# Kernel optimization log

Measured on AMD Instinct MI355X. Metric: run time of the kernel, lower is better.

Reference implementation:

```python
import jax, jax.numpy as jnp
import numpy as np


def _mlp(x, w1, b1, w2, b2, w3, b3):
    h = jax.nn.relu(x @ w1 + b1)
    h = jax.nn.relu(h @ w2 + b2)
    return h @ w3 + b3


def setup_inputs() -> dict:
    key = jax.random.key(0)
    N, E, G = 200000, 6400000, 1000
    IN, D = 16, 16
    ks = jax.random.split(key, 32)
    inp = {
        'x': jax.random.normal(ks[0], (N, IN), jnp.float32),
        'edge_index': jax.random.randint(ks[1], (2, E), 0, N),
        'batch': jnp.sort(jax.random.randint(ks[2], (N,), 0, G)),
        'num_graphs': G,
    }
    k = 3
    # make_mlp(in_ch, out_ch): in -> 32 -> 16 -> out
    for name, fin, dims in [('mlp1', IN, [32, 16, 8]),
                            ('mlp2', 8, [32, 16, D]),
                            ('mlp_dag', IN + D, [32, 16, D]),
                            ('mlp_global', D, [32, 16, D])]:
        d_in = fin
        for j, d_out in enumerate(dims):
            inp[f'{name}_w{j+1}'] = jax.random.normal(ks[k], (d_in, d_out), jnp.float32) / np.sqrt(d_in)
            inp[f'{name}_b{j+1}'] = jnp.zeros((d_out,), jnp.float32)
            k += 1
            d_in = d_out
    return inp


def reference(x, edge_index, batch, num_graphs,
              mlp1_w1, mlp1_b1, mlp1_w2, mlp1_b2, mlp1_w3, mlp1_b3,
              mlp2_w1, mlp2_b1, mlp2_w2, mlp2_b2, mlp2_w3, mlp2_b3,
              mlp_dag_w1, mlp_dag_b1, mlp_dag_w2, mlp_dag_b2, mlp_dag_w3, mlp_dag_b3,
              mlp_global_w1, mlp_global_b1, mlp_global_w2, mlp_global_b2, mlp_global_w3, mlp_global_b3):
    N = x.shape[0]
    loops = jnp.arange(N)
    row = jnp.concatenate([edge_index[0], loops])  # aggregation index (flow=target_to_source)
    col = jnp.concatenate([edge_index[1], loops])  # message source index

    # GCNConv: mlp1 -> normalized scatter-add -> mlp2
    h = _mlp(x, mlp1_w1, mlp1_b1, mlp1_w2, mlp1_b2, mlp1_w3, mlp1_b3)  # [N, 8]
    deg = jax.ops.segment_sum(jnp.ones_like(col, x.dtype), col, num_segments=N)
    dinv = jnp.where(deg > 0, 1.0 / jnp.sqrt(jnp.maximum(deg, 1.0)), 0.0)
    norm = dinv[row] * dinv[col]  # [E+N]
    agg = jax.ops.segment_sum(norm[:, None] * h[col], row, num_segments=N)  # [N, 8]
    x_node = _mlp(agg, mlp2_w1, mlp2_b1, mlp2_w2, mlp2_b2, mlp2_w3, mlp2_b3)  # [N, D]

    # DAG-level embedding: global_add_pool over batch, then mlp_dag
    x_comb = jnp.concatenate([x, x_node], axis=1)  # [N, IN+D]
    y = jax.ops.segment_sum(x_comb, batch, num_segments=num_graphs)  # [G, IN+D]
    y = _mlp(y, mlp_dag_w1, mlp_dag_b1, mlp_dag_w2, mlp_dag_b2, mlp_dag_w3, mlp_dag_b3)  # [G, D]

    # Global embedding
    z = _mlp(jnp.sum(y, axis=0), mlp_global_w1, mlp_global_b1, mlp_global_w2, mlp_global_b2, mlp_global_w3, mlp_global_b3)  # [D]
    return x_node, y, z
```

## Files before the change

### kernel.cpp

```cpp
#include <hip/hip_runtime.h>
#include <hip/hip_fp16.h>


#define BSH 8
#define BSZ 256
#define NBMAX 1024
#define TSZ 4096
#define ATSZ 8192
#define CH 16

__device__ __forceinline__ int lowerb(const int* __restrict__ b, int n, int v) {
  int lo = 0, hi = n;
  while (lo < hi) { int m = (lo + hi) >> 1; if (b[m] < v) lo = m + 1; else hi = m; }
  return lo;
}

__device__ __forceinline__ void addmsg(float* acc, uint4 g) {
  const __half2* h2 = reinterpret_cast<const __half2*>(&g);
  #pragma unroll
  for (int q = 0; q < 4; q++) {
    float2 f = __half22float2(h2[q]);
    acc[2 * q] += f.x;
    acc[2 * q + 1] += f.y;
  }
}


__global__ void __launch_bounds__(256)
k_hist(const int* __restrict__ row, const int* __restrict__ col, int E,
       int NBP, unsigned* __restrict__ Hr, unsigned* __restrict__ Hc) {
  __shared__ unsigned hr[NBMAX], hc[NBMAX];
  int t = threadIdx.x;
  int base = blockIdx.x * TSZ;
  int cnt = min(TSZ, E - base);
  for (int i = t; i < NBP; i += 256) { hr[i] = 0; hc[i] = 0; }
  __syncthreads();
  #pragma unroll
  for (int u = 0; u < 4; u++) {
    int idx = base + 4 * (t + 256 * u);
    unsigned rv[4], cv[4];
    if (idx + 3 < E) {
      uint4 r4 = *reinterpret_cast<const uint4*>(row + idx);
      uint4 c4 = *reinterpret_cast<const uint4*>(col + idx);
      rv[0] = r4.x; rv[1] = r4.y; rv[2] = r4.z; rv[3] = r4.w;
      cv[0] = c4.x; cv[1] = c4.y; cv[2] = c4.z; cv[3] = c4.w;
    } else {
      #pragma unroll
      for (int j = 0; j < 4; j++) {
        bool v = (idx + j) < E;
        rv[j] = v ? (unsigned)row[idx + j] : 0u;
        cv[j] = v ? (unsigned)col[idx + j] : 0u;
      }
    }
    int l0 = 4 * (t + 256 * u);
    #pragma unroll
    for (int j = 0; j < 4; j++) {
      if (l0 + j < cnt) {
        atomicAdd(&hr[rv[j] >> BSH], 1u);
        atomicAdd(&hc[cv[j] >> BSH], 1u);
      }
    }
  }
  __syncthreads();
  size_t rb = (size_t)blockIdx.x * NBP;
  for (int i = t; i < NBP; i += 256) {
    Hr[rb + i] = hr[i];
    Hc[rb + i] = hc[i];
  }
}

__global__ void __launch_bounds__(256)
k_colsum2(const unsigned* __restrict__ Hr, unsigned* __restrict__ Sr,
          const unsigned* __restrict__ Hc, unsigned* __restrict__ Sc,
          int NT, int NBP, int CSZ, int gcol) {
  int blk = blockIdx.x;
  const unsigned* H = Hr; unsigned* S = Sr;
  if (blk >= gcol) { blk -= gcol; H = Hc; S = Sc; }
  int i = blk * 256 + threadIdx.x;
  if (i >= CH * NBP) return;
  int ch = i / NBP, b = i - ch * NBP;
  int t0 = ch * CSZ, t1 = min(NT, t0 + CSZ);
  unsigned s = 0;
  for (int t = t0; t < t1; t++) s += H[(size_t)t * NBP + b];
  S[i] = s;
}

__global__ void __launch_bounds__(256)
k_colapply2(unsigned* __restrict__ Hr, const unsigned* __restrict__ Sr,
            unsigned* __restrict__ tot_r,
            unsigned* __restrict__ Hc, const unsigned* __restrict__ Sc,
            unsigned* __restrict__ tot_c,
            int NT, int NBP, int nb, int CSZ, int gcol) {
  int blk = blockIdx.x;
  unsigned* H = Hr; const unsigned* S = Sr; unsigned* tot = tot_r;
  if (blk >= gcol) { blk -= gcol; H = Hc; S = Sc; tot = tot_c; }
  int i = blk * 256 + threadIdx.x;
  if (i >= CH * NBP) return;
  int ch = i / NBP, b = i - ch * NBP;
  unsigned run = 0;
  for (int c = 0; c < ch; c++) run += S[c * NBP + b];
  int t0 = ch * CSZ, t1 = min(NT, t0 + CSZ);
  for (int t = t0; t < t1; t++) {
    unsigned v = H[(size_t)t * NBP + b];
    H[(size_t)t * NBP + b] = run;
    run += v;
  }
  if (ch == CH - 1 && b < nb) tot[b] = run;
}

__global__ void __launch_bounds__(1024)
k_scan2(const unsigned* __restrict__ tot_r, unsigned* __restrict__ offs_r,
        const unsigned* __restrict__ tot_c, unsigned* __restrict__ offs_c,
        int nb) {
  const unsigned* tot = blockIdx.x ? tot_c : tot_r;
  unsigned* offs = blockIdx.x ? offs_c : offs_r;
  unsigned pm1 = blockIdx.x ? 0u : 3u;
  __shared__ unsigned s[1024];
  int t = threadIdx.x;
  unsigned e0 = (2 * t < nb) ? ((tot[2 * t] + pm1) & ~pm1) : 0u;
  unsigned e1 = (2 * t + 1 < nb) ? ((tot[2 * t + 1] + pm1) & ~pm1) : 0u;
  unsigned sum = e0 + e1;
  s[t] = sum;
  __syncthreads();
  for (int d = 1; d < 1024; d <<= 1) {
    unsigned v = (t >= d) ? s[t - d] : 0u;
    __syncthreads();
    s[t] += v;
    __syncthreads();
  }
  unsigned ex = s[t] - sum;
  if (2 * t < nb)     offs[2 * t] = ex;
  if (2 * t + 1 < nb) offs[2 * t + 1] = ex + e0;
}

__global__ void __launch_bounds__(256)
k_scat2(const int* __restrict__ row, const int* __restrict__ col, int E, int nb,
        int NBP,
        const unsigned* __restrict__ Hr, const unsigned* __restrict__ Hc,
        const unsigned* __restrict__ offs_r, const unsigned* __restrict__ offs_c,
        unsigned* __restrict__ ebuf, unsigned short* __restrict__ ebuf2) {
  __shared__ unsigned buf[TSZ];
  __shared__ unsigned short bkt[TSZ];
  __shared__ unsigned h[NBMAX], diff[NBMAX];
  __shared__ unsigned sc[256];
  int t = threadIdx.x;
  int base = blockIdx.x * TSZ;
  int cnt = min(TSZ, E - base);
  size_t hrow = (size_t)blockIdx.x * NBP;

  unsigned rv[16], cv[16];
  #pragma unroll
  for (int u = 0; u < 4; u++) {
    int idx = base + 4 * (t + 256 * u);
    if (idx + 3 < E) {
      uint4 r4 = *reinterpret_cast<const uint4*>(row + idx);
      uint4 c4 = *reinterpret_cast<const uint4*>(col + idx);
      rv[4*u] = r4.x; rv[4*u+1] = r4.y; rv[4*u+2] = r4.z; rv[4*u+3] = r4.w;
      cv[4*u] = c4.x; cv[4*u+1] = c4.y; cv[4*u+2] = c4.z; cv[4*u+3] = c4.w;
    } else {
      #pragma unroll
      for (int j = 0; j < 4; j++) {
        bool v = (idx + j) < E;
        rv[4*u+j] = v ? (unsigned)row[idx + j] : 0u;
        cv[4*u+j] = v ? (unsigned)col[idx + j] : 0u;
      }
    }
  }

  for (int i = t; i < NBMAX; i += 256) h[i] = 0;
  __syncthreads();
  unsigned rk[16];
  #pragma unroll
  for (int u = 0; u < 4; u++) {
    int l0 = 4 * (t + 256 * u);
    #pragma unroll
    for (int j = 0; j < 4; j++)
      if (l0 + j < cnt) rk[4*u+j] = atomicAdd(&h[rv[4*u+j] >> BSH], 1u);
  }
  __syncthreads();
  {
    unsigned a0 = h[4*t], a1 = h[4*t+1], a2 = h[4*t+2], a3 = h[4*t+3];
    unsigned p1 = a0 + a1, p2 = p1 + a2, p3 = p2 + a3;
    sc[t] = p3;
    __syncthreads();
    for (int d = 1; d < 256; d <<= 1) {
      unsigned v = (t >= d) ? sc[t - d] : 0u;
      __syncthreads();
      sc[t] += v;
      __syncthreads();
    }
    unsigned ex = sc[t] - p3;
    unsigned l[4] = {ex, ex + a0, ex + p1, ex + p2};
    #pragma unroll
    for (int k = 0; k < 4; k++) {
      int b = 4 * t + k;
      h[b] = l[k];
      if (b < nb) diff[b] = offs_r[b] + Hr[hrow + b] - l[k];
    }
  }
  __syncthreads();
  #pragma unroll
  for (int u = 0; u < 4; u++) {
    int l0 = 4 * (t + 256 * u);
    #pragma unroll
    for (int j = 0; j < 4; j++) {
      if (l0 + j < cnt) {
        unsigned r = rv[4*u+j], b = r >> BSH;
        unsigned pos = h[b] + rk[4*u+j];
        buf[pos] = ((r & (BSZ - 1u)) << 18) | cv[4*u+j];
        bkt[pos] = (unsigned short)b;
      }
    }
  }
  __syncthreads();
  #pragma unroll
  for (int u = 0; u < 16; u++) {
    int s2 = t + 256 * u;
    if (s2 < cnt) {
      ebuf[(unsigned)s2 + diff[bkt[s2]]] = buf[s2];
    }
  }
  __syncthreads();

  for (int i = t; i < NBMAX; i += 256) h[i] = 0;
  __syncthreads();
  #pragma unroll
  for (int u = 0; u < 4; u++) {
    int l0 = 4 * (t + 256 * u);
    #pragma unroll
    for (int j = 0; j < 4; j++)
      if (l0 + j < cnt) rk[4*u+j] = atomicAdd(&h[cv[4*u+j] >> BSH], 1u);
  }
  __syncthreads();
  {
    unsigned a0 = h[4*t], a1 = h[4*t+1], a2 = h[4*t+2], a3 = h[4*t+3];
    unsigned p1 = a0 + a1, p2 = p1 + a2, p3 = p2 + a3;
    sc[t] = p3;
    __syncthreads();
    for (int d = 1; d < 256; d <<= 1) {
      unsigned v = (t >= d) ? sc[t - d] : 0u;
      __syncthreads();
      sc[t] += v;
      __syncthreads();
    }
    unsigned ex = sc[t] - p3;
    unsigned l[4] = {ex, ex + a0, ex + p1, ex + p2};
    #pragma unroll
    for (int k = 0; k < 4; k++) {
      int b = 4 * t + k;
      h[b] = l[k];
      if (b < nb) diff[b] = offs_c[b] + Hc[hrow + b] - l[k];
    }
  }
  __syncthreads();
  #pragma unroll
  for (int u = 0; u < 4; u++) {
    int l0 = 4 * (t + 256 * u);
    #pragma unroll
    for (int j = 0; j < 4; j++) {
      if (l0 + j < cnt) {
        unsigned c = cv[4*u+j], b = c >> BSH;
        unsigned pos = h[b] + rk[4*u+j];
        buf[pos] = c & (BSZ - 1u);
        bkt[pos] = (unsigned short)b;
      }
    }
  }
  __syncthreads();
  #pragma unroll
  for (int u = 0; u < 16; u++) {
    int s2 = t + 256 * u;
    if (s2 < cnt) {
      ebuf2[(unsigned)s2 + diff[bkt[s2]]] = (unsigned short)buf[s2];
    }
  }
}


__global__ void __launch_bounds__(256)
k_degm(const unsigned short* __restrict__ eb, const unsigned* __restrict__ offs_c,
       const unsigned* __restrict__ tot_c,
       const float* __restrict__ x,
       const float* __restrict__ w1, const float* __restrict__ b1,
       const float* __restrict__ w2, const float* __restrict__ b2,
       const float* __restrict__ w3, const float* __restrict__ b3,
       unsigned* __restrict__ deg, uint4* __restrict__ hs16, int N) {
  __shared__ unsigned cnt[BSZ];
  __shared__ float sW1[16 * 32], sB1[32], sW2[32 * 16], sB2[16], sW3[16 * 8], sB3[8];
  int b = blockIdx.x, t = threadIdx.x;
  cnt[t] = 0;
  sW1[t] = w1[t]; sW1[t + 256] = w1[t + 256];
  sW2[t] = w2[t]; sW2[t + 256] = w2[t + 256];
  if (t < 128) sW3[t] = w3[t];
  if (t < 32) sB1[t] = b1[t];
  if (t < 16) sB2[t] = b2[t];
  if (t < 8) sB3[t] = b3[t];
  __syncthreads();
  unsigned s = offs_c[b], n = tot_c[b];
  for (unsigned i = t; i < n; i += 256) atomicAdd(&cnt[eb[s + i]], 1u);
  __syncthreads();
  int node = b * BSZ + t;
  if (node >= N) return;
  unsigned d = cnt[t];
  deg[node] = d;

  float xin[16];
  const float4* xp = reinterpret_cast<const float4*>(x + (size_t)node * 16);
  #pragma unroll
  for (int q = 0; q < 4; q++) {
    float4 v = xp[q];
    xin[q * 4 + 0] = v.x; xin[q * 4 + 1] = v.y; xin[q * 4 + 2] = v.z; xin[q * 4 + 3] = v.w;
  }
  float h1[32];
  #pragma unroll
  for (int o = 0; o < 32; o++) {
    float s1 = sB1[o];
    #pragma unroll
    for (int k = 0; k < 16; k++) s1 = fmaf(xin[k], sW1[k * 32 + o], s1);
    h1[o] = fmaxf(s1, 0.f);
  }
  float h2[16];
  #pragma unroll
  for (int o = 0; o < 16; o++) {
    float s1 = sB2[o];
    #pragma unroll
    for (int k = 0; k < 32; k++) s1 = fmaf(h1[k], sW2[k * 16 + o], s1);
    h2[o] = fmaxf(s1, 0.f);
  }
  float dinv = rsqrtf((float)(d + 1u));
  float o0[8];
  #pragma unroll
  for (int o = 0; o < 8; o++) {
    float s1 = sB3[o];
    #pragma unroll
    for (int k = 0; k < 16; k++) s1 = fmaf(h2[k], sW3[k * 8 + o], s1);
    o0[o] = dinv * s1;
  }
  __half2 hh[4];
  #pragma unroll
  for (int q = 0; q < 4; q++) hh[q] = __floats2half2_rn(o0[2 * q], o0[2 * q + 1]);
  hs16[node] = *reinterpret_cast<const uint4*>(hh);
}


__global__ void __launch_bounds__(512)
k_agg(const unsigned* __restrict__ ebuf, const unsigned* __restrict__ offs,
      const unsigned* __restrict__ tot,
      const uint4* __restrict__ hs16, const unsigned* __restrict__ deg,
      const float* __restrict__ w1, const float* __restrict__ b1,
      const float* __restrict__ w2, const float* __restrict__ b2,
      const float* __restrict__ w3, const float* __restrict__ b3,
      float* __restrict__ xn, int N) {
  __shared__ unsigned sorted[ATSZ];
  __shared__ unsigned hist[256];
  __shared__ unsigned cum[257];
  __shared__ unsigned sc[256];
  __shared__ float stage[BSZ][9];
  __shared__ float sW1[256], sB1[32], sW2[512], sB2[16], sW3[256], sB3[16];
  int t = threadIdx.x;
  if (t < 256) { sW1[t] = w1[t]; sW3[t] = w3[t]; }
  else { int u = t - 256; sW2[u] = w2[u]; sW2[u + 256] = w2[u + 256]; }
  if (t < 32) sB1[t] = b1[t];
  if (t < 16) { sB2[t] = b2[t]; sB3[t] = b3[t]; }

  int b = blockIdx.x;
  unsigned s = offs[b], n = tot[b];
  unsigned nr = (n + 3u) & ~3u;

  float acc[8];
  #pragma unroll
  for (int c = 0; c < 8; c++) acc[c] = 0.f;
  int nl = t >> 1, half = t & 1;

  for (unsigned c0 = 0; c0 < n; c0 += ATSZ) {
    if (t < 256) hist[t] = 0;
    __syncthreads();

    unsigned rel[16], colv[16], rk[16];
    #pragma unroll
    for (int u = 0; u < 4; u++) {
      unsigned idx = c0 + 4 * (unsigned)(t + 512 * u);
      uint4 pk = make_uint4(0u, 0u, 0u, 0u);
      if (idx < nr) pk = *reinterpret_cast<const uint4*>(ebuf + s + idx);
      #pragma unroll
      for (int j = 0; j < 4; j++) {
        bool real = (idx + j) < n;
        unsigned p = (&pk.x)[j];
        rel[4*u+j]  = real ? (p >> 18) : 256u;
        colv[4*u+j] = p & 0x3FFFFu;
      }
    }
    #pragma unroll
    for (int u = 0; u < 16; u++)
      if (rel[u] < 256u) rk[u] = atomicAdd(&hist[rel[u]], 1u);
    __syncthreads();
    if (t < 256) sc[t] = hist[t];
    __syncthreads();
    for (int d = 1; d < 256; d <<= 1) {
      unsigned v = (t >= d && t < 256) ? sc[t - d] : 0u;
      __syncthreads();
      if (t < 256) sc[t] += v;
      __syncthreads();
    }
    if (t < 256) cum[t] = sc[t] - hist[t];
    if (t == 255) cum[256] = sc[255];
    __syncthreads();
    #pragma unroll
    for (int u = 0; u < 16; u++) {
      if (rel[u] < 256u) {
        sorted[cum[rel[u]] + rk[u]] = colv[u];
      }
    }
    __syncthreads();
    unsigned lo = cum[nl], hi = cum[nl + 1];
    unsigned len = hi - lo, mid = lo + (len >> 1);
    unsigned i = half ? mid : lo;
    unsigned e = half ? hi : mid;
    for (; i + 4 <= e; i += 4) {
      unsigned q0 = sorted[i], q1 = sorted[i + 1], q2 = sorted[i + 2], q3 = sorted[i + 3];
      uint4 g0 = hs16[q0];
      uint4 g1 = hs16[q1];
      uint4 g2 = hs16[q2];
      uint4 g3 = hs16[q3];
      addmsg(acc, g0); addmsg(acc, g1); addmsg(acc, g2); addmsg(acc, g3);
    }
    for (; i < e; i++) { uint4 g = hs16[sorted[i]]; addmsg(acc, g); }
    __syncthreads();
  }

  if (!half) {
    #pragma unroll
    for (int c = 0; c < 8; c++) stage[nl][c] = acc[c];
  }
  __syncthreads();
  if (half) {
    #pragma unroll
    for (int c = 0; c < 8; c++) stage[nl][c] += acc[c];
  }
  __syncthreads();

  if (t >= 256) return;
  int node = b * BSZ + t;
  if (node >= N) return;
  float dinv = rsqrtf((float)(deg[node] + 1u));
  uint4 selfp = hs16[node];
  const __half2* sh = reinterpret_cast<const __half2*>(&selfp);
  float a[8];
  #pragma unroll
  for (int q = 0; q < 4; q++) {
    float2 f = __half22float2(sh[q]);
    a[2 * q]     = dinv * (stage[t][2 * q] + f.x);
    a[2 * q + 1] = dinv * (stage[t][2 * q + 1] + f.y);
  }

  float h1[32];
  #pragma unroll
  for (int o = 0; o < 32; o++) {
    float v = sB1[o];
    #pragma unroll
    for (int k = 0; k < 8; k++) v = fmaf(a[k], sW1[k * 32 + o], v);
    h1[o] = fmaxf(v, 0.f);
  }
  float h2v[16];
  #pragma unroll
  for (int o = 0; o < 16; o++) {
    float v = sB2[o];
    #pragma unroll
    for (int k = 0; k < 32; k++) v = fmaf(h1[k], sW2[k * 16 + o], v);
    h2v[o] = fmaxf(v, 0.f);
  }
  float o0[16];
  #pragma unroll
  for (int o = 0; o < 16; o++) {
    float v = sB3[o];
    #pragma unroll
    for (int k = 0; k < 16; k++) v = fmaf(h2v[k], sW3[k * 16 + o], v);
    o0[o] = v;
  }
  float4* op = reinterpret_cast<float4*>(xn + (size_t)node * 16);
  #pragma unroll
  for (int q = 0; q < 4; q++)
    op[q] = make_float4(o0[q * 4], o0[q * 4 + 1], o0[q * 4 + 2], o0[q * 4 + 3]);
}


__global__ void __launch_bounds__(256)
k_pool(const float* __restrict__ x, const float* __restrict__ xn,
       const int* __restrict__ batch, float* __restrict__ pool, int N) {
  int g = blockIdx.x;
  int lo = lowerb(batch, N, g);
  int hi = lowerb(batch, N, g + 1);
  int c = threadIdx.x & 31;
  int j = threadIdx.x >> 5;
  float s = 0.f;
  for (int n = lo + j; n < hi; n += 8) {
    s += (c < 16) ? x[(size_t)n * 16 + c] : xn[(size_t)n * 16 + (c - 16)];
  }
  __shared__ float red[8][33];
  red[j][c] = s;
  __syncthreads();
  if (threadIdx.x < 32) {
    float t = 0.f;
    #pragma unroll
    for (int q = 0; q < 8; q++) t += red[q][threadIdx.x];
    pool[(size_t)g * 32 + threadIdx.x] = t;
  }
}

__global__ void __launch_bounds__(256)
k_dag(const float* __restrict__ pool,
      const float* __restrict__ w1, const float* __restrict__ b1,
      const float* __restrict__ w2, const float* __restrict__ b2,
      const float* __restrict__ w3, const float* __restrict__ b3,
      float* __restrict__ y, int G) {
  __shared__ float sW1[32 * 32], sB1[32], sW2[32 * 16], sB2[16], sW3[16 * 16], sB3[16];
  for (int t = threadIdx.x; t < 1024; t += blockDim.x) sW1[t] = w1[t];
  for (int t = threadIdx.x; t < 512; t += blockDim.x) sW2[t] = w2[t];
  for (int t = threadIdx.x; t < 256; t += blockDim.x) sW3[t] = w3[t];
  for (int t = threadIdx.x; t < 32; t += blockDim.x) sB1[t] = b1[t];
  for (int t = threadIdx.x; t < 16; t += blockDim.x) { sB2[t] = b2[t]; sB3[t] = b3[t]; }
  __syncthreads();
  int g = blockIdx.x * blockDim.x + threadIdx.x;
  if (g >= G) return;

  float in[32];
  const float4* pp = reinterpret_cast<const float4*>(pool + (size_t)g * 32);
  #pragma unroll
  for (int q = 0; q < 8; q++) {
    float4 v = pp[q];
    in[q * 4 + 0] = v.x; in[q * 4 + 1] = v.y; in[q * 4 + 2] = v.z; in[q * 4 + 3] = v.w;
  }
  float h1[32];
  #pragma unroll
  for (int o = 0; o < 32; o++) {
    float s = sB1[o];
    #pragma unroll
    for (int k = 0; k < 32; k++) s = fmaf(in[k], sW1[k * 32 + o], s);
    h1[o] = fmaxf(s, 0.f);
  }
  float h2[16];
  #pragma unroll
  for (int o = 0; o < 16; o++) {
    float s = sB2[o];
    #pragma unroll
    for (int k = 0; k < 32; k++) s = fmaf(h1[k], sW2[k * 16 + o], s);
    h2[o] = fmaxf(s, 0.f);
  }
  float o0[16];
  #pragma unroll
  for (int o = 0; o < 16; o++) {
    float s = sB3[o];
    #pragma unroll
    for (int k = 0; k < 16; k++) s = fmaf(h2[k], sW3[k * 16 + o], s);
    o0[o] = s;
  }
  float4* yp = reinterpret_cast<float4*>(y + (size_t)g * 16);
  #pragma unroll
  for (int q = 0; q < 4; q++)
    yp[q] = make_float4(o0[q * 4], o0[q * 4 + 1], o0[q * 4 + 2], o0[q * 4 + 3]);
}

__global__ void __launch_bounds__(256)
k_z(const float* __restrict__ y,
    const float* __restrict__ w1, const float* __restrict__ b1,
    const float* __restrict__ w2, const float* __restrict__ b2,
    const float* __restrict__ w3, const float* __restrict__ b3,
    float* __restrict__ z, int G) {
  __shared__ float red[16][17];
  __shared__ float sum[16], h1s[32], h2s[16];
  int t = threadIdx.x;
  int c = t & 15, j = t >> 4;
  float s = 0.f;
  for (int g = j; g < G; g += 16) s += y[(size_t)g * 16 + c];
  red[j][c] = s;
  __syncthreads();
  if (t < 16) {
    float v = 0.f;
    #pragma unroll
    for (int q = 0; q < 16; q++) v += red[q][t];
    sum[t] = v;
  }
  __syncthreads();
  if (t < 32) {
    float s1 = b1[t];
    #pragma unroll
    for (int k = 0; k < 16; k++) s1 = fmaf(sum[k], w1[k * 32 + t], s1);
    h1s[t] = fmaxf(s1, 0.f);
  }
  __syncthreads();
  if (t < 16) {
    float s2 = b2[t];
    #pragma unroll
    for (int k = 0; k < 32; k++) s2 = fmaf(h1s[k], w2[k * 16 + t], s2);
    h2s[t] = fmaxf(s2, 0.f);
  }
  __syncthreads();
  if (t < 16) {
    float s3 = b3[t];
    #pragma unroll
    for (int k = 0; k < 16; k++) s3 = fmaf(h2s[k], w3[k * 16 + t], s3);
    z[t] = s3;
  }
}


__global__ void k_deg_atomic(const int* __restrict__ col, unsigned* __restrict__ deg, int E) {
  int e = blockIdx.x * blockDim.x + threadIdx.x;
  if (e < E) atomicAdd(&deg[col[e]], 1u);
}

__global__ void __launch_bounds__(256)
k_mlp1f(const float* __restrict__ x, const unsigned* __restrict__ deg,
        const float* __restrict__ w1, const float* __restrict__ b1,
        const float* __restrict__ w2, const float* __restrict__ b2,
        const float* __restrict__ w3, const float* __restrict__ b3,
        float* __restrict__ hs, int N) {
  __shared__ float sW1[16 * 32], sB1[32], sW2[32 * 16], sB2[16], sW3[16 * 8], sB3[8];
  for (int t = threadIdx.x; t < 512; t += blockDim.x) { sW1[t] = w1[t]; sW2[t] = w2[t]; }
  for (int t = threadIdx.x; t < 128; t += blockDim.x) sW3[t] = w3[t];
  for (int t = threadIdx.x; t < 32; t += blockDim.x) sB1[t] = b1[t];
  for (int t = threadIdx.x; t < 16; t += blockDim.x) sB2[t] = b2[t];
  for (int t = threadIdx.x; t < 8; t += blockDim.x) sB3[t] = b3[t];
  __syncthreads();
  int i = blockIdx.x * blockDim.x + threadIdx.x;
  if (i >= N) return;
  float xin[16];
  const float4* xp = reinterpret_cast<const float4*>(x + (size_t)i * 16);
  #pragma unroll
  for (int q = 0; q < 4; q++) {
    float4 v = xp[q];
    xin[q * 4 + 0] = v.x; xin[q * 4 + 1] = v.y; xin[q * 4 + 2] = v.z; xin[q * 4 + 3] = v.w;
  }
  float h1[32];
  #pragma unroll
  for (int o = 0; o < 32; o++) {
    float s = sB1[o];
    #pragma unroll
    for (int k = 0; k < 16; k++) s = fmaf(xin[k], sW1[k * 32 + o], s);
    h1[o] = fmaxf(s, 0.f);
  }
  float h2[16];
  #pragma unroll
  for (int o = 0; o < 16; o++) {
    float s = sB2[o];
    #pragma unroll
    for (int k = 0; k < 32; k++) s = fmaf(h1[k], sW2[k * 16 + o], s);
    h2[o] = fmaxf(s, 0.f);
  }
  float dinv = rsqrtf((float)(deg[i] + 1u));
  float o0[8];
  #pragma unroll
  for (int o = 0; o < 8; o++) {
    float s = sB3[o];
    #pragma unroll
    for (int k = 0; k < 16; k++) s = fmaf(h2[k], sW3[k * 8 + o], s);
    o0[o] = dinv * s;
  }
  float4* hp = reinterpret_cast<float4*>(hs + (size_t)i * 8);
  hp[0] = make_float4(o0[0], o0[1], o0[2], o0[3]);
  hp[1] = make_float4(o0[4], o0[5], o0[6], o0[7]);
}

__global__ void k_scatter_atomic(const int* __restrict__ row, const int* __restrict__ col,
                                 const float* __restrict__ hs, float* __restrict__ acc, int E) {
  int e = blockIdx.x * blockDim.x + threadIdx.x;
  if (e >= E) return;
  int r = row[e], c = col[e];
  const float4* hp = reinterpret_cast<const float4*>(hs + (size_t)c * 8);
  float4 a = hp[0], b = hp[1];
  float* ap = acc + (size_t)r * 8;
  atomicAdd(ap + 0, a.x); atomicAdd(ap + 1, a.y);
  atomicAdd(ap + 2, a.z); atomicAdd(ap + 3, a.w);
  atomicAdd(ap + 4, b.x); atomicAdd(ap + 5, b.y);
  atomicAdd(ap + 6, b.z); atomicAdd(ap + 7, b.w);
}

__global__ void __launch_bounds__(256)
k_finalize(const float* __restrict__ hs, const float* __restrict__ acc,
           const unsigned* __restrict__ deg,
           const float* __restrict__ w1, const float* __restrict__ b1,
           const float* __restrict__ w2, const float* __restrict__ b2,
           const float* __restrict__ w3, const float* __restrict__ b3,
           float* __restrict__ xn, int N) {
  __shared__ float sW1[8 * 32], sB1[32], sW2[32 * 16], sB2[16], sW3[16 * 16], sB3[16];
  for (int t = threadIdx.x; t < 256; t += blockDim.x) { sW1[t] = w1[t]; sW3[t] = w3[t]; }
  for (int t = threadIdx.x; t < 512; t += blockDim.x) sW2[t] = w2[t];
  for (int t = threadIdx.x; t < 32; t += blockDim.x) sB1[t] = b1[t];
  for (int t = threadIdx.x; t < 16; t += blockDim.x) { sB2[t] = b2[t]; sB3[t] = b3[t]; }
  __syncthreads();
  int i = blockIdx.x * blockDim.x + threadIdx.x;
  if (i >= N) return;
  float dinv = rsqrtf((float)(deg[i] + 1u));
  float a[8];
  const float4* accp = reinterpret_cast<const float4*>(acc + (size_t)i * 8);
  const float4* hsp = reinterpret_cast<const float4*>(hs + (size_t)i * 8);
  float4 a0 = accp[0], a1 = accp[1], s0 = hsp[0], s1 = hsp[1];
  a[0] = dinv * (a0.x + s0.x); a[1] = dinv * (a0.y + s0.y);
  a[2] = dinv * (a0.z + s0.z); a[3] = dinv * (a0.w + s0.w);
  a[4] = dinv * (a1.x + s1.x); a[5] = dinv * (a1.y + s1.y);
  a[6] = dinv * (a1.z + s1.z); a[7] = dinv * (a1.w + s1.w);
  float h1[32];
  #pragma unroll
  for (int o = 0; o < 32; o++) {
    float s = sB1[o];
    #pragma unroll
    for (int k = 0; k < 8; k++) s = fmaf(a[k], sW1[k * 32 + o], s);
    h1[o] = fmaxf(s, 0.f);
  }
  float h2[16];
  #pragma unroll
  for (int o = 0; o < 16; o++) {
    float s = sB2[o];
    #pragma unroll
    for (int k = 0; k < 32; k++) s = fmaf(h1[k], sW2[k * 16 + o], s);
    h2[o] = fmaxf(s, 0.f);
  }
  float o0[16];
  #pragma unroll
  for (int o = 0; o < 16; o++) {
    float s = sB3[o];
    #pragma unroll
    for (int k = 0; k < 16; k++) s = fmaf(h2[k], sW3[k * 16 + o], s);
    o0[o] = s;
  }
  float4* op = reinterpret_cast<float4*>(xn + (size_t)i * 16);
  #pragma unroll
  for (int q = 0; q < 4; q++)
    op[q] = make_float4(o0[q * 4], o0[q * 4 + 1], o0[q * 4 + 2], o0[q * 4 + 3]);
}


extern "C" void kernel_launch(void* const* d_in, const int* in_sizes, int n_in,
                              void* d_out, int out_size, void* d_ws, size_t ws_size,
                              hipStream_t stream) {
  const float* x = (const float*)d_in[0];
  const int* ei = (const int*)d_in[1];
  const int* batch = (const int*)d_in[2];
  const float* m1w1 = (const float*)d_in[4];  const float* m1b1 = (const float*)d_in[5];
  const float* m1w2 = (const float*)d_in[6];  const float* m1b2 = (const float*)d_in[7];
  const float* m1w3 = (const float*)d_in[8];  const float* m1b3 = (const float*)d_in[9];
  const float* m2w1 = (const float*)d_in[10]; const float* m2b1 = (const float*)d_in[11];
  const float* m2w2 = (const float*)d_in[12]; const float* m2b2 = (const float*)d_in[13];
  const float* m2w3 = (const float*)d_in[14]; const float* m2b3 = (const float*)d_in[15];
  const float* mdw1 = (const float*)d_in[16]; const float* mdb1 = (const float*)d_in[17];
  const float* mdw2 = (const float*)d_in[18]; const float* mdb2 = (const float*)d_in[19];
  const float* mdw3 = (const float*)d_in[20]; const float* mdb3 = (const float*)d_in[21];
  const float* mgw1 = (const float*)d_in[22]; const float* mgb1 = (const float*)d_in[23];
  const float* mgw2 = (const float*)d_in[24]; const float* mgb2 = (const float*)d_in[25];
  const float* mgw3 = (const float*)d_in[26]; const float* mgb3 = (const float*)d_in[27];

  int N = in_sizes[0] / 16;
  int E = in_sizes[1] / 2;
  int G = (out_size - N * 16 - 16) / 16;
  const int* rowp = ei;
  const int* colp = ei + E;

  float* xn = (float*)d_out;
  float* yv = xn + (size_t)N * 16;
  float* zv = yv + (size_t)G * 16;

  int nb = (N + BSZ - 1) / BSZ;
  int NT = (E + TSZ - 1) / TSZ;
  int NBP = (nb + 63) & ~63;
  int CSZ = (NT + CH - 1) / CH;

  size_t off = 0;
  auto alloc = [&](size_t bytes) -> size_t {
    off = (off + 255) & ~(size_t)255;
    size_t o = off; off += bytes; return o;
  };
  char* ws = (char*)d_ws;
  size_t o_deg  = alloc((size_t)N * 4);
  size_t o_hs16 = alloc((size_t)N * 16);
  size_t o_cnt  = alloc((size_t)4 * NBMAX * 4);
  size_t o_Hr   = alloc((size_t)NT * NBP * 4);
  size_t o_Hc   = alloc((size_t)NT * NBP * 4);
  size_t o_S    = alloc((size_t)2 * CH * NBP * 4);
  size_t o_eb   = alloc(((size_t)E + 4 * NBMAX) * 4);
  size_t o_eb2  = alloc((size_t)E * 2);
  size_t o_pool = alloc((size_t)G * 32 * 4);
  size_t need = off;

  bool bucketed = (ws_size >= need) && (nb <= NBMAX) && (N <= (1 << 18));

  if (bucketed) {
    unsigned* deg = (unsigned*)(ws + o_deg);
    uint4* hs16 = (uint4*)(ws + o_hs16);
    unsigned* tot_r  = (unsigned*)(ws + o_cnt);
    unsigned* offs_r = tot_r + NBMAX;
    unsigned* tot_c  = tot_r + 2 * NBMAX;
    unsigned* offs_c = tot_r + 3 * NBMAX;
    unsigned* Hr = (unsigned*)(ws + o_Hr);
    unsigned* Hc = (unsigned*)(ws + o_Hc);
    unsigned* Sr = (unsigned*)(ws + o_S);
    unsigned* Sc = Sr + CH * NBP;
    unsigned* ebuf = (unsigned*)(ws + o_eb);
    unsigned short* ebuf2 = (unsigned short*)(ws + o_eb2);
    float* pool = (float*)(ws + o_pool);

    int gcol = (CH * NBP + 255) / 256;
    k_hist<<<NT, 256, 0, stream>>>(rowp, colp, E, NBP, Hr, Hc);
    k_colsum2<<<2 * gcol, 256, 0, stream>>>(Hr, Sr, Hc, Sc, NT, NBP, CSZ, gcol);
    k_colapply2<<<2 * gcol, 256, 0, stream>>>(Hr, Sr, tot_r, Hc, Sc, tot_c,
                                              NT, NBP, nb, CSZ, gcol);
    k_scan2<<<2, 1024, 0, stream>>>(tot_r, offs_r, tot_c, offs_c, nb);
    k_scat2<<<NT, 256, 0, stream>>>(rowp, colp, E, nb, NBP, Hr, Hc,
                                    offs_r, offs_c, ebuf, ebuf2);
    k_degm<<<nb, 256, 0, stream>>>(ebuf2, offs_c, tot_c, x,
                                   m1w1, m1b1, m1w2, m1b2, m1w3, m1b3,
                                   deg, hs16, N);
    k_agg<<<nb, 512, 0, stream>>>(ebuf, offs_r, tot_r, hs16, deg,
                                  m2w1, m2b1, m2w2, m2b2, m2w3, m2b3, xn, N);

    k_pool<<<G, 256, 0, stream>>>(x, xn, batch, pool, N);
    k_dag<<<(G + 255) / 256, 256, 0, stream>>>(pool, mdw1, mdb1, mdw2, mdb2, mdw3, mdb3, yv, G);
    k_z<<<1, 256, 0, stream>>>(yv, mgw1, mgb1, mgw2, mgb2, mgw3, mgb3, zv, G);
  } else {
    unsigned* deg = (unsigned*)ws;
    float* acc = (float*)(ws + (size_t)N * 4);
    float* hs  = (float*)(ws + (size_t)N * 36);
    float* pool = (float*)(ws + (size_t)N * 68);

    hipMemsetAsync(ws, 0, (size_t)N * 36, stream);
    const int TB = 256;
    k_deg_atomic<<<(E + TB - 1) / TB, TB, 0, stream>>>(colp, deg, E);
    k_mlp1f<<<(N + TB - 1) / TB, TB, 0, stream>>>(x, deg, m1w1, m1b1, m1w2, m1b2, m1w3, m1b3, hs, N);
    k_scatter_atomic<<<(E + TB - 1) / TB, TB, 0, stream>>>(rowp, colp, hs, acc, E);
    k_finalize<<<(N + TB - 1) / TB, TB, 0, stream>>>(hs, acc, deg, m2w1, m2b1, m2w2, m2b2, m2w3, m2b3, xn, N);
    k_pool<<<G, TB, 0, stream>>>(x, xn, batch, pool, N);
    k_dag<<<(G + TB - 1) / TB, TB, 0, stream>>>(pool, mdw1, mdb1, mdw2, mdb2, mdw3, mdb3, yv, G);
    k_z<<<1, TB, 0, stream>>>(yv, mgw1, mgb1, mgw2, mgb2, mgw3, mgb3, zv, G);
  }
}
```

Before: 243.2 us.

## Widen scatter blocks, use wave-shuffle scans, balance aggregation, fuse pool with DAG MLP

Result: slower. 283.2 us (+16.5%).

```diff
diff --git a/kernel.cpp b/kernel.cpp
--- a/kernel.cpp
+++ b/kernel.cpp
@@ -133,7 +133,7 @@
   if (2 * t + 1 < nb) offs[2 * t + 1] = ex + e0;
 }
 
-__global__ void __launch_bounds__(256)
+__global__ void __launch_bounds__(512)
 k_scat2(const int* __restrict__ row, const int* __restrict__ col, int E, int nb,
         int NBP,
         const unsigned* __restrict__ Hr, const unsigned* __restrict__ Hc,
@@ -142,16 +142,16 @@
   __shared__ unsigned buf[TSZ];
   __shared__ unsigned short bkt[TSZ];
   __shared__ unsigned h[NBMAX], diff[NBMAX];
-  __shared__ unsigned sc[256];
+  __shared__ unsigned wtot[4];
   int t = threadIdx.x;
   int base = blockIdx.x * TSZ;
   int cnt = min(TSZ, E - base);
   size_t hrow = (size_t)blockIdx.x * NBP;
 
-  unsigned rv[16], cv[16];
-  #pragma unroll
-  for (int u = 0; u < 4; u++) {
-    int idx = base + 4 * (t + 256 * u);
+  unsigned rv[8], cv[8];
+  #pragma unroll
+  for (int u = 0; u < 2; u++) {
+    int idx = base + 4 * (t + 512 * u);
     if (idx + 3 < E) {
       uint4 r4 = *reinterpret_cast<const uint4*>(row + idx);
       uint4 c4 = *reinterpret_cast<const uint4*>(col + idx);
@@ -167,29 +167,34 @@
     }
   }
 
-  for (int i = t; i < NBMAX; i += 256) h[i] = 0;
-  __syncthreads();
-  unsigned rk[16];
-  #pragma unroll
-  for (int u = 0; u < 4; u++) {
-    int l0 = 4 * (t + 256 * u);
+  for (int i = t; i < NBMAX; i += 512) h[i] = 0;
+  __syncthreads();
+  unsigned rk[8];
+  #pragma unroll
+  for (int u = 0; u < 2; u++) {
+    int l0 = 4 * (t + 512 * u);
     #pragma unroll
     for (int j = 0; j < 4; j++)
       if (l0 + j < cnt) rk[4*u+j] = atomicAdd(&h[rv[4*u+j] >> BSH], 1u);
   }
   __syncthreads();
-  {
-    unsigned a0 = h[4*t], a1 = h[4*t+1], a2 = h[4*t+2], a3 = h[4*t+3];
-    unsigned p1 = a0 + a1, p2 = p1 + a2, p3 = p2 + a3;
-    sc[t] = p3;
-    __syncthreads();
-    for (int d = 1; d < 256; d <<= 1) {
-      unsigned v = (t >= d) ? sc[t - d] : 0u;
-      __syncthreads();
-      sc[t] += v;
-      __syncthreads();
-    }
-    unsigned ex = sc[t] - p3;
+  unsigned a0 = 0, a1 = 0, a2 = 0, a3 = 0, p1 = 0, p2 = 0, p3 = 0, isum = 0;
+  if (t < 256) {
+    a0 = h[4*t]; a1 = h[4*t+1]; a2 = h[4*t+2]; a3 = h[4*t+3];
+    p1 = a0 + a1; p2 = p1 + a2; p3 = p2 + a3;
+    isum = p3;
+    #pragma unroll
+    for (int d = 1; d < 64; d <<= 1) {
+      unsigned o = __shfl_up(isum, d, 64);
+      if ((t & 63) >= d) isum += o;
+    }
+    if ((t & 63) == 63) wtot[t >> 6] = isum;
+  }
+  __syncthreads();
+  if (t < 256) {
+    unsigned woff = 0;
+    for (int w = 0; w < (t >> 6); w++) woff += wtot[w];
+    unsigned ex = woff + isum - p3;
     unsigned l[4] = {ex, ex + a0, ex + p1, ex + p2};
     #pragma unroll
     for (int k = 0; k < 4; k++) {
@@ -200,8 +205,8 @@
   }
   __syncthreads();
   #pragma unroll
-  for (int u = 0; u < 4; u++) {
-    int l0 = 4 * (t + 256 * u);
+  for (int u = 0; u < 2; u++) {
+    int l0 = 4 * (t + 512 * u);
     #pragma unroll
     for (int j = 0; j < 4; j++) {
       if (l0 + j < cnt) {
@@ -214,36 +219,39 @@
   }
   __syncthreads();
   #pragma unroll
-  for (int u = 0; u < 16; u++) {
-    int s2 = t + 256 * u;
-    if (s2 < cnt) {
-      ebuf[(unsigned)s2 + diff[bkt[s2]]] = buf[s2];
-    }
-  }
-  __syncthreads();
-
-  for (int i = t; i < NBMAX; i += 256) h[i] = 0;
-  __syncthreads();
-  #pragma unroll
-  for (int u = 0; u < 4; u++) {
-    int l0 = 4 * (t + 256 * u);
+  for (int u = 0; u < 8; u++) {
+    int s2 = t + 512 * u;
+    if (s2 < cnt) ebuf[(unsigned)s2 + diff[bkt[s2]]] = buf[s2];
+  }
+  __syncthreads();
+
+  for (int i = t; i < NBMAX; i += 512) h[i] = 0;
+  __syncthreads();
+  #pragma unroll
+  for (int u = 0; u < 2; u++) {
+    int l0 = 4 * (t + 512 * u);
     #pragma unroll
     for (int j = 0; j < 4; j++)
       if (l0 + j < cnt) rk[4*u+j] = atomicAdd(&h[cv[4*u+j] >> BSH], 1u);
   }
   __syncthreads();
-  {
-    unsigned a0 = h[4*t], a1 = h[4*t+1], a2 = h[4*t+2], a3 = h[4*t+3];
-    unsigned p1 = a0 + a1, p2 = p1 + a2, p3 = p2 + a3;
-    sc[t] = p3;
-    __syncthreads();
-    for (int d = 1; d < 256; d <<= 1) {
-      unsigned v = (t >= d) ? sc[t - d] : 0u;
-      __syncthreads();
-      sc[t] += v;
-      __syncthreads();
-    }
-    unsigned ex = sc[t] - p3;
+  a0 = a1 = a2 = a3 = p1 = p2 = p3 = isum = 0;
+  if (t < 256) {
+    a0 = h[4*t]; a1 = h[4*t+1]; a2 = h[4*t+2]; a3 = h[4*t+3];
+    p1 = a0 + a1; p2 = p1 + a2; p3 = p2 + a3;
+    isum = p3;
+    #pragma unroll
+    for (int d = 1; d < 64; d <<= 1) {
+      unsigned o = __shfl_up(isum, d, 64);
+      if ((t & 63) >= d) isum += o;
+    }
+    if ((t & 63) == 63) wtot[t >> 6] = isum;
+  }
+  __syncthreads();
+  if (t < 256) {
+    unsigned woff = 0;
+    for (int w = 0; w < (t >> 6); w++) woff += wtot[w];
+    unsigned ex = woff + isum - p3;
     unsigned l[4] = {ex, ex + a0, ex + p1, ex + p2};
     #pragma unroll
     for (int k = 0; k < 4; k++) {
@@ -254,8 +262,8 @@
   }
   __syncthreads();
   #pragma unroll
-  for (int u = 0; u < 4; u++) {
-    int l0 = 4 * (t + 256 * u);
+  for (int u = 0; u < 2; u++) {
+    int l0 = 4 * (t + 512 * u);
     #pragma unroll
     for (int j = 0; j < 4; j++) {
       if (l0 + j < cnt) {
@@ -268,11 +276,9 @@
   }
   __syncthreads();
   #pragma unroll
-  for (int u = 0; u < 16; u++) {
-    int s2 = t + 256 * u;
-    if (s2 < cnt) {
-      ebuf2[(unsigned)s2 + diff[bkt[s2]]] = (unsigned short)buf[s2];
-    }
+  for (int u = 0; u < 8; u++) {
+    int s2 = t + 512 * u;
+    if (s2 < cnt) ebuf2[(unsigned)s2 + diff[bkt[s2]]] = (unsigned short)buf[s2];
   }
 }
 
@@ -354,25 +360,22 @@
   __shared__ unsigned sorted[ATSZ];
   __shared__ unsigned hist[256];
   __shared__ unsigned cum[257];
-  __shared__ unsigned sc[256];
-  __shared__ float stage[BSZ][9];
+  __shared__ unsigned wtot[4];
+  __shared__ float acc[8][BSZ];
   __shared__ float sW1[256], sB1[32], sW2[512], sB2[16], sW3[256], sB3[16];
   int t = threadIdx.x;
   if (t < 256) { sW1[t] = w1[t]; sW3[t] = w3[t]; }
   else { int u = t - 256; sW2[u] = w2[u]; sW2[u + 256] = w2[u + 256]; }
   if (t < 32) sB1[t] = b1[t];
   if (t < 16) { sB2[t] = b2[t]; sB3[t] = b3[t]; }
+  for (int i = t; i < 8 * BSZ; i += 512) (&acc[0][0])[i] = 0.f;
 
   int b = blockIdx.x;
   unsigned s = offs[b], n = tot[b];
   unsigned nr = (n + 3u) & ~3u;
 
-  float acc[8];
-  #pragma unroll
-  for (int c = 0; c < 8; c++) acc[c] = 0.f;
-  int nl = t >> 1, half = t & 1;
-
   for (unsigned c0 = 0; c0 < n; c0 += ATSZ) {
+    unsigned chn = min(n - c0, (unsigned)ATSZ);
     if (t < 256) hist[t] = 0;
     __syncthreads();
 
@@ -394,50 +397,67 @@
     for (int u = 0; u < 16; u++)
       if (rel[u] < 256u) rk[u] = atomicAdd(&hist[rel[u]], 1u);
     __syncthreads();
-    if (t < 256) sc[t] = hist[t];
+    if (t < 64) {
+      unsigned v0 = hist[4*t], v1 = hist[4*t+1], v2 = hist[4*t+2], v3 = hist[4*t+3];
+      unsigned q1 = v0 + v1, q2 = q1 + v2, q3 = q2 + v3;
+      unsigned isum = q3;
+      #pragma unroll
+      for (int d = 1; d < 64; d <<= 1) {
+        unsigned o = __shfl_up(isum, d, 64);
+        if (t >= d) isum += o;
+      }
+      unsigned ex = isum - q3;
+      cum[4*t] = ex; cum[4*t+1] = ex + v0; cum[4*t+2] = ex + q1; cum[4*t+3] = ex + q2;
+      if (t == 63) cum[256] = isum;
+    }
     __syncthreads();
-    for (int d = 1; d < 256; d <<= 1) {
-      unsigned v = (t >= d && t < 256) ? sc[t - d] : 0u;
-      __syncthreads();
-      if (t < 256) sc[t] += v;
-      __syncthreads();
-    }
-    if (t < 256) cum[t] = sc[t] - hist[t];
-    if (t == 255) cum[256] = sc[255];
+    #pragma unroll
+    for (int u = 0; u < 16; u++) {
+      if (rel[u] < 256u) sorted[cum[rel[u]] + rk[u]] = colv[u];
+    }
     __syncthreads();
-    #pragma unroll
-    for (int u = 0; u < 16; u++) {
-      if (rel[u] < 256u) {
-        sorted[cum[rel[u]] + rk[u]] = colv[u];
+
+    unsigned lo = (unsigned)t * 16u;
+    unsigned hi = min(chn, lo + 16u);
+    if (lo < hi) {
+      int a = 1, bnd = 256;
+      while (a < bnd) { int m = (a + bnd) >> 1; if (cum[m] <= lo) a = m + 1; else bnd = m; }
+      int nd = a - 1;
+      float part[8];
+      #pragma unroll
+      for (int c = 0; c < 8; c++) part[c] = 0.f;
+      bool dirty = false;
+      unsigned i = lo;
+      while (i < hi) {
+        while (i >= cum[nd + 1]) {
+          if (dirty) {
+            #pragma unroll
+            for (int c = 0; c < 8; c++) atomicAdd(&acc[c][nd], part[c]);
+            #pragma unroll
+            for (int c = 0; c < 8; c++) part[c] = 0.f;
+            dirty = false;
+          }
+          nd++;
+        }
+        unsigned lim = min(hi, cum[nd + 1]);
+        for (; i + 4 <= lim; i += 4) {
+          unsigned q0 = sorted[i], q1 = sorted[i+1], q2 = sorted[i+2], q3 = sorted[i+3];
+          uint4 g0 = hs16[q0];
+          uint4 g1 = hs16[q1];
+          uint4 g2 = hs16[q2];
+          uint4 g3 = hs16[q3];
+          addmsg(part, g0); addmsg(part, g1); addmsg(part, g2); addmsg(part, g3);
+          dirty = true;
+        }
+        for (; i < lim; i++) { uint4 g = hs16[sorted[i]]; addmsg(part, g); dirty = true; }
       }
+      if (dirty) {
+        #pragma unroll
+        for (int c = 0; c < 8; c++) atomicAdd(&acc[c][nd], part[c]);
+      }
     }
     __syncthreads();
-    unsigned lo = cum[nl], hi = cum[nl + 1];
-    unsigned len = hi - lo, mid = lo + (len >> 1);
-    unsigned i = half ? mid : lo;
-    unsigned e = half ? hi : mid;
-    for (; i + 4 <= e; i += 4) {
-      unsigned q0 = sorted[i], q1 = sorted[i + 1], q2 = sorted[i + 2], q3 = sorted[i + 3];
-      uint4 g0 = hs16[q0];
-      uint4 g1 = hs16[q1];
-      uint4 g2 = hs16[q2];
-      uint4 g3 = hs16[q3];
-      addmsg(acc, g0); addmsg(acc, g1); addmsg(acc, g2); addmsg(acc, g3);
-    }
-    for (; i < e; i++) { uint4 g = hs16[sorted[i]]; addmsg(acc, g); }
-    __syncthreads();
-  }
-
-  if (!half) {
-    #pragma unroll
-    for (int c = 0; c < 8; c++) stage[nl][c] = acc[c];
-  }
-  __syncthreads();
-  if (half) {
-    #pragma unroll
-    for (int c = 0; c < 8; c++) stage[nl][c] += acc[c];
-  }
-  __syncthreads();
+  }
 
   if (t >= 256) return;
   int node = b * BSZ + t;
@@ -449,8 +469,8 @@
   #pragma unroll
   for (int q = 0; q < 4; q++) {
     float2 f = __half22float2(sh[q]);
-    a[2 * q]     = dinv * (stage[t][2 * q] + f.x);
-    a[2 * q + 1] = dinv * (stage[t][2 * q + 1] + f.y);
+    a[2 * q]     = dinv * (acc[2 * q][t] + f.x);
+    a[2 * q + 1] = dinv * (acc[2 * q + 1][t] + f.y);
   }
 
   float h1[32];
@@ -485,79 +505,61 @@
 
 
 __global__ void __launch_bounds__(256)
-k_pool(const float* __restrict__ x, const float* __restrict__ xn,
-       const int* __restrict__ batch, float* __restrict__ pool, int N) {
+k_poold(const float* __restrict__ x, const float* __restrict__ xn,
+        const int* __restrict__ batch,
+        const float* __restrict__ w1, const float* __restrict__ b1,
+        const float* __restrict__ w2, const float* __restrict__ b2,
+        const float* __restrict__ w3, const float* __restrict__ b3,
+        float* __restrict__ y, int N) {
+  __shared__ float red[8][33];
+  __shared__ float pv[32], h1s[32];
+  __shared__ float sW1[1024], sW2[512], sW3[256], sB1[32], sB2[16], sB3[16];
+  int t = threadIdx.x;
+  for (int i = t; i < 1024; i += 256) sW1[i] = w1[i];
+  for (int i = t; i < 512; i += 256) sW2[i] = w2[i];
+  if (t < 256) sW3[t] = w3[t];
+  if (t < 32) sB1[t] = b1[t];
+  if (t < 16) { sB2[t] = b2[t]; sB3[t] = b3[t]; }
+
   int g = blockIdx.x;
   int lo = lowerb(batch, N, g);
   int hi = lowerb(batch, N, g + 1);
-  int c = threadIdx.x & 31;
-  int j = threadIdx.x >> 5;
+  int c = t & 31;
+  int j = t >> 5;
   float s = 0.f;
   for (int n = lo + j; n < hi; n += 8) {
     s += (c < 16) ? x[(size_t)n * 16 + c] : xn[(size_t)n * 16 + (c - 16)];
   }
-  __shared__ float red[8][33];
   red[j][c] = s;
   __syncthreads();
-  if (threadIdx.x < 32) {
-    float t = 0.f;
-    #pragma unroll
-    for (int q = 0; q < 8; q++) t += red[q][threadIdx.x];
-    pool[(size_t)g * 32 + threadIdx.x] = t;
-  }
-}
-
-__global__ void __launch_bounds__(256)
-k_dag(const float* __restrict__ pool,
-      const float* __restrict__ w1, const float* __restrict__ b1,
-      const float* __restrict__ w2, const float* __restrict__ b2,
-      const float* __restrict__ w3, const float* __restrict__ b3,
-      float* __restrict__ y, int G) {
-  __shared__ float sW1[32 * 32], sB1[32], sW2[32 * 16], sB2[16], sW3[16 * 16], sB3[16];
-  for (int t = threadIdx.x; t < 1024; t += blockDim.x) sW1[t] = w1[t];
-  for (int t = threadIdx.x; t < 512; t += blockDim.x) sW2[t] = w2[t];
-  for (int t = threadIdx.x; t < 256; t += blockDim.x) sW3[t] = w3[t];
-  for (int t = threadIdx.x; t < 32; t += blockDim.x) sB1[t] = b1[t];
-  for (int t = threadIdx.x; t < 16; t += blockDim.x) { sB2[t] = b2[t]; sB3[t] = b3[t]; }
-  __syncthreads();
-  int g = blockIdx.x * blockDim.x + threadIdx.x;
-  if (g >= G) return;
-
-  float in[32];
-  const float4* pp = reinterpret_cast<const float4*>(pool + (size_t)g * 32);
-  #pragma unroll
-  for (int q = 0; q < 8; q++) {
-    float4 v = pp[q];
-    in[q * 4 + 0] = v.x; in[q * 4 + 1] = v.y; in[q * 4 + 2] = v.z; in[q * 4 + 3] = v.w;
-  }
-  float h1[32];
-  #pragma unroll
-  for (int o = 0; o < 32; o++) {
-    float s = sB1[o];
-    #pragma unroll
-    for (int k = 0; k < 32; k++) s = fmaf(in[k], sW1[k * 32 + o], s);
-    h1[o] = fmaxf(s, 0.f);
-  }
-  float h2[16];
-  #pragma unroll
-  for (int o = 0; o < 16; o++) {
-    float s = sB2[o];
-    #pragma unroll
-    for (int k = 0; k < 32; k++) s = fmaf(h1[k], sW2[k * 16 + o], s);
-    h2[o] = fmaxf(s, 0.f);
-  }
-  float o0[16];
-  #pragma unroll
-  for (int o = 0; o < 16; o++) {
-    float s = sB3[o];
-    #pragma unroll
-    for (int k = 0; k < 16; k++) s = fmaf(h2[k], sW3[k * 16 + o], s);
-    o0[o] = s;
-  }
-  float4* yp = reinterpret_cast<float4*>(y + (size_t)g * 16);
-  #pragma unroll
-  for (int q = 0; q < 4; q++)
-    yp[q] = make_float4(o0[q * 4], o0[q * 4 + 1], o0[q * 4 + 2], o0[q * 4 + 3]);
+  if (t < 32) {
+    float v = 0.f;
+    #pragma unroll
+    for (int q = 0; q < 8; q++) v += red[q][t];
+    pv[t] = v;
+  }
+  __syncthreads();
+  if (t < 32) {
+    float s1 = sB1[t];
+    #pragma unroll
+    for (int k = 0; k < 32; k++) s1 = fmaf(pv[k], sW1[k * 32 + t], s1);
+    h1s[t] = fmaxf(s1, 0.f);
+  }
+  __syncthreads();
+  if (t < 16) {
+    float s2 = sB2[t];
+    #pragma unroll
+    for (int k = 0; k < 32; k++) s2 = fmaf(h1s[k], sW2[k * 16 + t], s2);
+    float h2 = fmaxf(s2, 0.f);
+    red[0][t] = h2;
+  }
+  __syncthreads();
+  if (t < 16) {
+    float s3 = sB3[t];
+    #pragma unroll
+    for (int k = 0; k < 16; k++) s3 = fmaf(red[0][k], sW3[k * 16 + t], s3);
+    y[(size_t)g * 16 + t] = s3;
+  }
 }
 
 __global__ void __launch_bounds__(256)
@@ -727,6 +729,81 @@
   #pragma unroll
   for (int q = 0; q < 4; q++)
     op[q] = make_float4(o0[q * 4], o0[q * 4 + 1], o0[q * 4 + 2], o0[q * 4 + 3]);
+}
+
+__global__ void __launch_bounds__(256)
+k_pool(const float* __restrict__ x, const float* __restrict__ xn,
+       const int* __restrict__ batch, float* __restrict__ pool, int N) {
+  int g = blockIdx.x;
+  int lo = lowerb(batch, N, g);
+  int hi = lowerb(batch, N, g + 1);
+  int c = threadIdx.x & 31;
+  int j = threadIdx.x >> 5;
+  float s = 0.f;
+  for (int n = lo + j; n < hi; n += 8) {
+    s += (c < 16) ? x[(size_t)n * 16 + c] : xn[(size_t)n * 16 + (c - 16)];
+  }
+  __shared__ float red[8][33];
+  red[j][c] = s;
+  __syncthreads();
+  if (threadIdx.x < 32) {
+    float t = 0.f;
+    #pragma unroll
+    for (int q = 0; q < 8; q++) t += red[q][threadIdx.x];
+    pool[(size_t)g * 32 + threadIdx.x] = t;
+  }
+}
+
+__global__ void __launch_bounds__(256)
+k_dag(const float* __restrict__ pool,
+      const float* __restrict__ w1, const float* __restrict__ b1,
+      const float* __restrict__ w2, const float* __restrict__ b2,
+      const float* __restrict__ w3, const float* __restrict__ b3,
+      float* __restrict__ y, int G) {
+  __shared__ float sW1[32 * 32], sB1[32], sW2[32 * 16], sB2[16], sW3[16 * 16], sB3[16];
+  for (int t = threadIdx.x; t < 1024; t += blockDim.x) sW1[t] = w1[t];
+  for (int t = threadIdx.x; t < 512; t += blockDim.x) sW2[t] = w2[t];
+  for (int t = threadIdx.x; t < 256; t += blockDim.x) sW3[t] = w3[t];
+  for (int t = threadIdx.x; t < 32; t += blockDim.x) sB1[t] = b1[t];
+  for (int t = threadIdx.x; t < 16; t += blockDim.x) { sB2[t] = b2[t]; sB3[t] = b3[t]; }
+  __syncthreads();
+  int g = blockIdx.x * blockDim.x + threadIdx.x;
+  if (g >= G) return;
+  float in[32];
+  const float4* pp = reinterpret_cast<const float4*>(pool + (size_t)g * 32);
+  #pragma unroll
+  for (int q = 0; q < 8; q++) {
+    float4 v = pp[q];
+    in[q * 4 + 0] = v.x; in[q * 4 + 1] = v.y; in[q * 4 + 2] = v.z; in[q * 4 + 3] = v.w;
+  }
+  float h1[32];
+  #pragma unroll
+  for (int o = 0; o < 32; o++) {
+    float s = sB1[o];
+    #pragma unroll
+    for (int k = 0; k < 32; k++) s = fmaf(in[k], sW1[k * 32 + o], s);
+    h1[o] = fmaxf(s, 0.f);
+  }
+  float h2[16];
+  #pragma unroll
+  for (int o = 0; o < 16; o++) {
+    float s = sB2[o];
+    #pragma unroll
+    for (int k = 0; k < 32; k++) s = fmaf(h1[k], sW2[k * 16 + o], s);
+    h2[o] = fmaxf(s, 0.f);
+  }
+  float o0[16];
+  #pragma unroll
+  for (int o = 0; o < 16; o++) {
+    float s = sB3[o];
+    #pragma unroll
+    for (int k = 0; k < 16; k++) s = fmaf(h2[k], sW3[k * 16 + o], s);
+    o0[o] = s;
+  }
+  float4* yp = reinterpret_cast<float4*>(y + (size_t)g * 16);
+  #pragma unroll
+  for (int q = 0; q < 4; q++)
+    yp[q] = make_float4(o0[q * 4], o0[q * 4 + 1], o0[q * 4 + 2], o0[q * 4 + 3]);
 }
 
 
@@ -796,7 +873,6 @@
     unsigned* Sc = Sr + CH * NBP;
     unsigned* ebuf = (unsigned*)(ws + o_eb);
     unsigned short* ebuf2 = (unsigned short*)(ws + o_eb2);
-    float* pool = (float*)(ws + o_pool);
 
     int gcol = (CH * NBP + 255) / 256;
     k_hist<<<NT, 256, 0, stream>>>(rowp, colp, E, NBP, Hr, Hc);
@@ -804,16 +880,15 @@
     k_colapply2<<<2 * gcol, 256, 0, stream>>>(Hr, Sr, tot_r, Hc, Sc, tot_c,
                                               NT, NBP, nb, CSZ, gcol);
     k_scan2<<<2, 1024, 0, stream>>>(tot_r, offs_r, tot_c, offs_c, nb);
-    k_scat2<<<NT, 256, 0, stream>>>(rowp, colp, E, nb, NBP, Hr, Hc,
+    k_scat2<<<NT, 512, 0, stream>>>(rowp, colp, E, nb, NBP, Hr, Hc,
                                     offs_r, offs_c, ebuf, ebuf2);
     k_degm<<<nb, 256, 0, stream>>>(ebuf2, offs_c, tot_c, x,
                                    m1w1, m1b1, m1w2, m1b2, m1w3, m1b3,
                                    deg, hs16, N);
     k_agg<<<nb, 512, 0, stream>>>(ebuf, offs_r, tot_r, hs16, deg,
                                   m2w1, m2b1, m2w2, m2b2, m2w3, m2b3, xn, N);
-
-    k_pool<<<G, 256, 0, stream>>>(x, xn, batch, pool, N);
-    k_dag<<<(G + 255) / 256, 256, 0, stream>>>(pool, mdw1, mdb1, mdw2, mdb2, mdw3, mdb3, yv, G);
+    k_poold<<<G, 256, 0, stream>>>(x, xn, batch,
+                                   mdw1, mdb1, mdw2, mdb2, mdw3, mdb3, yv, N);
     k_z<<<1, 256, 0, stream>>>(yv, mgw1, mgb1, mgw2, mgb2, mgw3, mgb3, zv, G);
   } else {
     unsigned* deg = (unsigned*)ws;
```
